# Kernel optimization log

Measured on AMD Instinct MI355X. Metric: run time of the kernel, lower is better.

The kernel has to match this reference:

```python
import jax, jax.numpy as jnp
import numpy as np

TEMPERATURE = 0.07
TAU_THRESHOLD = 0.5

B, D, K = 32768, 512, 2048


def _l2_normalize(x, axis=-1, eps=1e-12):
    # matches torch F.normalize: x / max(||x||, eps)
    n = jnp.linalg.norm(x, axis=axis, keepdims=True)
    return x / jnp.maximum(n, eps)


def setup_inputs() -> dict:
    key = jax.random.key(0)
    k1, k2, k3, k4 = jax.random.split(key, 4)
    embeddings = jax.random.normal(k1, (B, D), dtype=jnp.float32)
    best_similarity = jax.random.uniform(k2, (B,), dtype=jnp.float32)
    global_prototypes = jax.random.normal(k3, (K, D), dtype=jnp.float32)
    prototype_confidence = jax.random.uniform(k4, (K,), dtype=jnp.float32)
    return {
        "embeddings": embeddings,
        "best_similarity": best_similarity,
        "global_prototypes": global_prototypes,
        "prototype_confidence": prototype_confidence,
    }


def reference(embeddings, best_similarity, global_prototypes, prototype_confidence):
    en = _l2_normalize(embeddings, axis=1)          # [B, D]
    pn = _l2_normalize(global_prototypes, axis=1)   # [K, D]
    sims = jnp.einsum("bd,kd->bk", en, pn)          # [B, K] cosine sims
    best_proto_idx = jnp.argmax(sims, axis=1)       # [B]

    logits = sims / TEMPERATURE
    log_probs = jax.nn.log_softmax(logits, axis=1)  # [B, K]
    probs = jnp.exp(log_probs)
    entropy = -jnp.sum(probs * log_probs, axis=1)   # [B]
    max_entropy = jnp.log(jnp.float32(K))
    entropy_norm = entropy / (max_entropy + 1e-8)
    tau_adaptive = TAU_THRESHOLD - 0.2 * entropy_norm

    # confidence_weighted gating
    batch_conf = prototype_confidence[best_proto_idx]                     # [B]
    sigmoid_gate = jax.nn.sigmoid((best_similarity - tau_adaptive) / TEMPERATURE)
    gate = batch_conf * sigmoid_gate                                      # [B]

    target_protos = pn[best_proto_idx]                                    # [B, D]
    dist = jnp.linalg.norm(en - target_protos, axis=1)                    # [B]
    L_proto = jnp.mean(gate * dist)
    return (L_proto, gate)
```

## Files before the change

kernel.cpp:

```cpp
#include <hip/hip_runtime.h>
#include <math.h>


#define NB 32768
#define ND 512
#define NK 2048
#define TEMPR 0.07f
#define INV_T 14.285714285714286f
#define DX 1.4285714e-4f

typedef unsigned short u16;
typedef unsigned long long u64;
using bf16x8 = __attribute__((ext_vector_type(8))) short;
using u16x8 = __attribute__((ext_vector_type(8))) unsigned short;
using f32x16 = __attribute__((ext_vector_type(16))) float;

__device__ inline u16 bf_hi(float x) {
  unsigned u = __float_as_uint(x);
  u = u + 0x7FFFu + ((u >> 16) & 1u);
  return (u16)(u >> 16);
}
__device__ inline float bf_tof(u16 h) {
  return __uint_as_float(((unsigned)h) << 16);
}
__device__ inline void gload_lds16(const void* g, void* l) {
  __builtin_amdgcn_global_load_lds((const __attribute__((address_space(1))) void*)g,
                                   (__attribute__((address_space(3))) void*)l, 16, 0, 0);
}
#define MF(a, b, c) __builtin_amdgcn_mfma_f32_32x32x16_bf16((a), (b), (c), 0, 0, 0)

#define WAIT_LGKM0 { asm volatile("s_waitcnt lgkmcnt(0)" ::: "memory"); \
                     __builtin_amdgcn_sched_barrier(0); }
#define WAIT_VM5   { asm volatile("s_waitcnt vmcnt(5)" ::: "memory"); \
                     __builtin_amdgcn_sched_barrier(0); }
#define SBAR       { __builtin_amdgcn_s_barrier(); \
                     __builtin_amdgcn_sched_barrier(0); }

__global__ __launch_bounds__(256) void kprep_p(const float* __restrict__ P,
                                               u16* __restrict__ Phi,
                                               u16* __restrict__ Plo,
                                               float* __restrict__ invp,
                                               int* __restrict__ cnt) {
  if (blockIdx.x == 0 && threadIdx.x == 0) *cnt = 0;
  const int lane = threadIdx.x & 63, w = threadIdx.x >> 6;
  const int p = blockIdx.x * 4 + w;
  const float4* pr = (const float4*)(P + (size_t)p * ND);
  float4 a = pr[2 * lane], b = pr[2 * lane + 1];
  float ss = a.x * a.x + a.y * a.y + a.z * a.z + a.w * a.w
           + b.x * b.x + b.y * b.y + b.z * b.z + b.w * b.w;
#pragma unroll
  for (int off = 32; off > 0; off >>= 1) ss += __shfl_xor(ss, off);
  const float inv = 1.0f / fmaxf(sqrtf(ss), 1e-12f);
  if (lane == 0) invp[p] = inv;
  u16x8 h8, l8;
#define PCNV(j, f) { float n_ = (f) * inv; u16 hb_ = bf_hi(n_); \
  h8[j] = hb_; l8[j] = bf_hi(n_ - bf_tof(hb_)); }
  PCNV(0, a.x) PCNV(1, a.y) PCNV(2, a.z) PCNV(3, a.w)
  PCNV(4, b.x) PCNV(5, b.y) PCNV(6, b.z) PCNV(7, b.w)
#undef PCNV
  const int kt = p >> 8, pl = p & 255;
  const size_t idx =
      ((size_t)((kt * 32 + (lane >> 1)) * 2 + (lane & 1)) * 256 + pl) * 8;
  *(u16x8*)(Phi + idx) = h8;
  *(u16x8*)(Plo + idx) = l8;
}

__global__ __launch_bounds__(256) void kprep_e2(const float* __restrict__ E,
                                                u16* __restrict__ Ehi,
                                                u16* __restrict__ Elo) {
  const int lane = threadIdx.x & 63, w = threadIdx.x >> 6;
  const int row = blockIdx.x * 4 + w;
  const float4* er = (const float4*)(E + (size_t)row * ND);
  float4 a = er[lane], b = er[lane + 64];
  float ss = a.x * a.x + a.y * a.y + a.z * a.z + a.w * a.w
           + b.x * b.x + b.y * b.y + b.z * b.z + b.w * b.w;
#pragma unroll
  for (int off = 32; off > 0; off >>= 1) ss += __shfl_xor(ss, off);
  const float inv = 1.0f / fmaxf(sqrtf(ss), 1e-12f);
  ushort4 h4, l4;
#define PCNV(dst_h, dst_l, f) { float n_ = (f) * inv; u16 hb_ = bf_hi(n_); \
  dst_h = hb_; dst_l = bf_hi(n_ - bf_tof(hb_)); }
  PCNV(h4.x, l4.x, a.x) PCNV(h4.y, l4.y, a.y) PCNV(h4.z, l4.z, a.z) PCNV(h4.w, l4.w, a.w)
  *(ushort4*)(Ehi + (size_t)row * ND + lane * 4) = h4;
  *(ushort4*)(Elo + (size_t)row * ND + lane * 4) = l4;
  PCNV(h4.x, l4.x, b.x) PCNV(h4.y, l4.y, b.y) PCNV(h4.z, l4.z, b.z) PCNV(h4.w, l4.w, b.w)
  *(ushort4*)(Ehi + (size_t)row * ND + (lane + 64) * 4) = h4;
  *(ushort4*)(Elo + (size_t)row * ND + (lane + 64) * 4) = l4;
#undef PCNV
}

#define UPD2S(i, vv, pp) { \
  float x_ = fmaf((vv), INV_T, -INV_T); \
  float e_ = __expf(x_); \
  sS[i] += e_; uS[i] = fmaf(x_, e_, uS[i]); \
  bool u1_ = x_ > mm1[i]; \
  float lo_ = u1_ ? mm1[i] : x_; \
  mm2[i] = fmaxf(mm2[i], lo_); \
  mm1[i] = u1_ ? x_ : mm1[i]; \
  ixx[i] = u1_ ? (pp) : ixx[i]; }

__global__ __launch_bounds__(256, 3) void kmain_v9(
    const float* __restrict__ BS,
    const u16* __restrict__ PhiG, const u16* __restrict__ PloG,
    const u16* __restrict__ EhiG, const u16* __restrict__ EloG,
    const float* __restrict__ CONF,
    float* __restrict__ tau_ws, float* __restrict__ gd, float* __restrict__ gate_out,
    int* __restrict__ cnt, int* __restrict__ flags, u64* __restrict__ pk) {
  __shared__ u16 Ahi[2][4096], Alo[2][4096];
  __shared__ u16 Bhi[2][1024], Blo[2][1024];

  const int t = threadIdx.x;
  const int lane = t & 63;
  const int w = t >> 6;
  const int wr = w & 1;
  const int wc = w >> 1;
  const int c = lane & 31, h = lane >> 5;
  const int swz = (blockIdx.x & 7) * 64 + (blockIdx.x >> 3);
  const int row0 = swz * 64;

  int aoff[2];
#pragma unroll
  for (int i = 0; i < 2; ++i) aoff[i] = ((w * 2 + i) * 64 + lane) * 8;

  const u16* Bsrc = ((w < 2) ? EhiG : EloG) + (size_t)(row0 + lane) * ND + (w & 1) * 8;
  const int bslot = ((w & 1) * 64 + lane) * 8;

  const int arb = (h * 256 + wr * 128 + c) * 8;
  const int bro = (h * 64 + wc * 32 + c) * 8;

  f32x16 acc0, acc1, acc2, acc3;
#pragma unroll
  for (int i = 0; i < 16; ++i) { acc0[i] = 0.f; acc1[i] = 0.f; acc2[i] = 0.f; acc3[i] = 0.f; }
  float sS[4], uS[4], mm1[4], mm2[4];
  int ixx[4];
#pragma unroll
  for (int i = 0; i < 4; ++i) {
    sS[i] = 0.f; uS[i] = 0.f; mm1[i] = -3.0e38f; mm2[i] = -3.0e38f; ixx[i] = 0;
  }

#define SA9(tile_u16, nx) { \
  _Pragma("unroll") \
  for (int i = 0; i < 2; ++i) { \
    gload_lds16(PhiG + (tile_u16) + aoff[i], &Ahi[nx][aoff[i]]); \
    gload_lds16(PloG + (tile_u16) + aoff[i], &Alo[nx][aoff[i]]); \
  } }
#define SB9(col, nx) { \
  if (w < 2) { gload_lds16(Bsrc + (col), &Bhi[nx][bslot]); } \
  else       { gload_lds16(Bsrc + (col), &Blo[nx][bslot]); } }

  SA9(0, 0);
  SB9(0, 0);
  SA9(4096, 1);
  SB9(16, 1);
  WAIT_VM5;
  SBAR;

#pragma unroll 2
  for (int step = 0; step < 256; ++step) {
    const int cur = step & 1;
    const bf16x8 bh = *(const bf16x8*)&Bhi[cur][bro];
    const bf16x8 bl = *(const bf16x8*)&Blo[cur][bro];
    const bf16x8 ah0 = *(const bf16x8*)&Ahi[cur][arb];
    const bf16x8 ah1 = *(const bf16x8*)&Ahi[cur][arb + 256];
    const bf16x8 ah2 = *(const bf16x8*)&Ahi[cur][arb + 512];
    const bf16x8 ah3 = *(const bf16x8*)&Ahi[cur][arb + 768];
    const bf16x8 al0 = *(const bf16x8*)&Alo[cur][arb];
    const bf16x8 al1 = *(const bf16x8*)&Alo[cur][arb + 256];
    const bf16x8 al2 = *(const bf16x8*)&Alo[cur][arb + 512];
    const bf16x8 al3 = *(const bf16x8*)&Alo[cur][arb + 768];

    acc0 = MF(ah0, bh, acc0); acc1 = MF(ah1, bh, acc1);
    acc2 = MF(ah2, bh, acc2); acc3 = MF(ah3, bh, acc3);

    WAIT_LGKM0;
    SBAR;

    const int ns = (step < 254) ? step + 2 : 255;
    SA9(ns * 4096, cur);
    SB9((ns & 31) * 16, cur);

    acc0 = MF(ah0, bl, acc0); acc1 = MF(ah1, bl, acc1);
    acc2 = MF(ah2, bl, acc2); acc3 = MF(ah3, bl, acc3);
    acc0 = MF(al0, bh, acc0); acc1 = MF(al1, bh, acc1);
    acc2 = MF(al2, bh, acc2); acc3 = MF(al3, bh, acc3);

    if ((step & 31) == 31) {
      const int pb = (step >> 5) * 256 + wr * 128 + 4 * h;
#define DIG(i, ACC) { \
  _Pragma("unroll") \
  for (int r = 0; r < 16; ++r) { \
    UPD2S(i, ACC[r], pb + (i)*32 + (r & 3) + 8 * (r >> 2)) \
    ACC[r] = 0.f; \
  } }
      DIG(0, acc0)
      DIG(1, acc1)
      DIG(2, acc2)
      DIG(3, acc3)
#undef DIG
    }

    WAIT_VM5;
    SBAR;
  }

  __syncthreads();

  float s = 0.f, u = 0.f, m = -3.0e38f, m2f = -3.0e38f;
  int idx = 0;
#pragma unroll
  for (int i = 0; i < 4; ++i) {
    s += sS[i]; u += uS[i];
    bool up = (mm1[i] > m) || (mm1[i] == m && ixx[i] < idx);
    m2f = fmaxf(m2f, mm2[i]);
    m2f = fmaxf(m2f, up ? m : mm1[i]);
    m = up ? mm1[i] : m;
    idx = up ? ixx[i] : idx;
  }

  {
    float mo = __shfl_xor(m, 32);
    float so = __shfl_xor(s, 32);
    float uo = __shfl_xor(u, 32);
    float m2o = __shfl_xor(m2f, 32);
    int io = __shfl_xor(idx, 32);
    s += so; u += uo;
    bool up = (mo > m) || (mo == m && io < idx);
    m2f = fmaxf(m2f, m2o);
    m2f = fmaxf(m2f, up ? m : mo);
    m = up ? mo : m;
    idx = up ? io : idx;
  }

  float* mg = (float*)&Ahi[0][0];
  if (lane < 32) {
    const int base = ((wc * 2 + wr) * 32 + c) * 6;
    mg[base + 0] = m;
    mg[base + 1] = s;
    mg[base + 2] = u;
    mg[base + 3] = __int_as_float(idx);
    mg[base + 4] = m2f;
  }
  __syncthreads();

  if (wr == 0 && lane < 32) {
    const int b0 = ((wc * 2 + 0) * 32 + lane) * 6;
    const int b1 = ((wc * 2 + 1) * 32 + lane) * 6;
    float m1a = mg[b0], s0 = mg[b0 + 1], u0 = mg[b0 + 2];
    int i0 = __float_as_int(mg[b0 + 3]);
    float m2a = mg[b0 + 4];
    float m1b = mg[b1], s1 = mg[b1 + 1], u1 = mg[b1 + 2];
    int i1 = __float_as_int(mg[b1 + 3]);
    float m2b = mg[b1 + 4];

    bool up = (m1b > m1a) || (m1b == m1a && i1 < i0);
    float mf = fmaxf(m1a, m1b);
    float m2ff = fmaxf(fmaxf(m2a, m2b), fminf(m1a, m1b));
    int idxf = up ? i1 : i0;
    bool flg = (mf - m2ff) < DX;
    float sf = s0 + s1, uf = u0 + u1;

    float ent = logf(sf) - uf / sf;
    float tau = 0.5f - 0.2f * (ent * (1.0f / (7.6246190071f + 1e-8f)));
    float simmax = fmaf(mf, TEMPR, 1.0f);
    float dist = sqrtf(fmaxf(2.0f - 2.0f * simmax, 0.0f));
    int grow = row0 + wc * 32 + lane;
    float g = CONF[idxf] / (1.0f + __expf(-(BS[grow] - tau) * INV_T));
    gate_out[grow] = g;
    gd[grow] = g * dist;
    tau_ws[grow] = tau;
    if (flg) {
      pk[grow] = 0ull;
      int p = atomicAdd(cnt, 1);
      flags[p] = grow;
    }
  }
}

__global__ __launch_bounds__(256) void krescore4(
    const float* __restrict__ E, const float* __restrict__ P,
    const float* __restrict__ invp, const int* __restrict__ cnt,
    const int* __restrict__ flags, u64* __restrict__ pk) {
  const int n = *cnt;
  const int total = n * 16;
  const int t = threadIdx.x;
  const int k = t & 15;
  const int G = t >> 4;

  for (int ch = blockIdx.x; ch < total; ch += gridDim.x) {
    const int j = ch >> 4, q = ch & 15;
    const int row = flags[j];
    float4 e[8];
    float ss = 0.f;
    const float4* er = (const float4*)(E + (size_t)row * ND);
#pragma unroll
    for (int i = 0; i < 8; ++i) {
      e[i] = er[k + 16 * i];
      ss += e[i].x * e[i].x + e[i].y * e[i].y + e[i].z * e[i].z + e[i].w * e[i].w;
    }
#pragma unroll
    for (int o = 1; o < 16; o <<= 1) ss += __shfl_xor(ss, o);
    const float inv = 1.0f / fmaxf(sqrtf(ss), 1e-12f);
#pragma unroll
    for (int i = 0; i < 8; ++i) {
      e[i].x *= inv; e[i].y *= inv; e[i].z *= inv; e[i].w *= inv;
    }

    float best = -3.0e38f;
    int bidx = NK;
#pragma unroll 2
    for (int m = 0; m < 8; ++m) {
      const int p = q * 128 + G + 16 * m;
      const float4* pr = (const float4*)(P + (size_t)p * ND);
      float dot = 0.f;
#pragma unroll
      for (int i = 0; i < 8; ++i) {
        float4 a = pr[k + 16 * i];
        dot = fmaf(a.x, e[i].x, dot); dot = fmaf(a.y, e[i].y, dot);
        dot = fmaf(a.z, e[i].z, dot); dot = fmaf(a.w, e[i].w, dot);
      }
#pragma unroll
      for (int o = 1; o < 16; o <<= 1) dot += __shfl_xor(dot, o);
      float sim = dot * invp[p];
      if (sim > best) { best = sim; bidx = p; }
    }
    if (k == 0) {
      unsigned u = __float_as_uint(best);
      unsigned ord = (u & 0x80000000u) ? ~u : (u | 0x80000000u);
      u64 v = ((u64)ord << 32) | (unsigned)(NK - bidx);
      atomicMax(pk + row, v);
    }
  }
}

__global__ __launch_bounds__(1024) void kreduce2(
    float* __restrict__ gd, const float* __restrict__ BS,
    const float* __restrict__ CONF, const float* __restrict__ tau_ws,
    const int* __restrict__ cnt, const int* __restrict__ flags,
    const u64* __restrict__ pk, float* __restrict__ out0,
    float* __restrict__ gate_out) {
  __shared__ float red[1024];
  const int t = threadIdx.x;

  const int n = *cnt;
  for (int j = t; j < n; j += 1024) {
    const int row = flags[j];
    const u64 v = pk[row];
    const unsigned hi = (unsigned)(v >> 32);
    const int idx = NK - (int)(v & 0xFFFFFFFFu);
    const float sim = (hi & 0x80000000u) ? __uint_as_float(hi & 0x7FFFFFFFu)
                                         : __uint_as_float(~hi);
    const float tau = tau_ws[row];
    const float dist = sqrtf(fmaxf(2.0f - 2.0f * sim, 0.0f));
    const float g = CONF[idx] / (1.0f + __expf(-(BS[row] - tau) * INV_T));
    gate_out[row] = g;
    gd[row] = g * dist;
  }
  __syncthreads();

  float s = 0.f;
  const float4* g4 = (const float4*)gd;
  for (int i = t; i < 8192; i += 1024) {
    float4 v = g4[i];
    s += (v.x + v.y) + (v.z + v.w);
  }
  red[t] = s;
  __syncthreads();
  for (int off = 512; off > 0; off >>= 1) {
    if (t < off) red[t] += red[t + off];
    __syncthreads();
  }
  if (t == 0) out0[0] = red[0] * (1.0f / 32768.0f);
}

extern "C" void kernel_launch(void* const* d_in, const int* in_sizes, int n_in,
                              void* d_out, int out_size, void* d_ws, size_t ws_size,
                              hipStream_t stream) {
  const float* E = (const float*)d_in[0];
  const float* BS = (const float*)d_in[1];
  const float* P = (const float*)d_in[2];
  const float* CONF = (const float*)d_in[3];
  float* out = (float*)d_out;

  char* wsb = (char*)d_ws;
  u16* Phi = (u16*)wsb;
  u16* Plo = (u16*)(wsb + ((size_t)2 << 20));
  u16* Ehi = (u16*)(wsb + ((size_t)4 << 20));
  u16* Elo = (u16*)(wsb + ((size_t)36 << 20));
  char* tail = wsb + ((size_t)68 << 20);
  float* tau_ws = (float*)tail;
  float* gd = (float*)(tail + 131072);
  int* flags = (int*)(tail + 2 * 131072);
  int* cnt = (int*)(tail + 3 * 131072);
  float* invp = (float*)(tail + 3 * 131072 + 4096);
  u64* pk = (u64*)(tail + 3 * 131072 + 4096 + 8192);

  kprep_p<<<512, 256, 0, stream>>>(P, Phi, Plo, invp, cnt);
  kprep_e2<<<8192, 256, 0, stream>>>(E, Ehi, Elo);
  kmain_v9<<<512, 256, 0, stream>>>(BS, Phi, Plo, Ehi, Elo, CONF, tau_ws, gd,
                                    out + 1, cnt, flags, pk);
  krescore4<<<2048, 256, 0, stream>>>(E, P, invp, cnt, flags, pk);
  kreduce2<<<1, 1024, 0, stream>>>(gd, BS, CONF, tau_ws, cnt, flags, pk,
                                   out, out + 1);
}
```

Before: 280.5 us.

## Split prototype dimension across two blocks and convert embeddings to bf16 in-kernel

The main GEMM kernel now splits the 2048 prototypes into two halves, launching 1024 blocks instead of 512. Each block writes partial softmax/argmax statistics, and a new merge kernel combines them and computes the gate. The embedding prep kernel now only computes inverse norms. The main kernel loads fp32 embeddings directly and converts them to hi/lo bf16 pairs into LDS each step, which removes the 64MB Ehi/Elo round-trip through global memory. In exchange it adds an extra launch, partial-result traffic, and VALU conversion work in the inner loop, and the embedding tile is reconverted by both halves.

```diff
diff --git a/kernel.cpp b/kernel.cpp
--- a/kernel.cpp
+++ b/kernel.cpp
@@ -65,9 +65,8 @@
   *(u16x8*)(Plo + idx) = l8;
 }
 
-__global__ __launch_bounds__(256) void kprep_e2(const float* __restrict__ E,
-                                                u16* __restrict__ Ehi,
-                                                u16* __restrict__ Elo) {
+__global__ __launch_bounds__(256) void kprep_e(const float* __restrict__ E,
+                                               float* __restrict__ inv_e) {
   const int lane = threadIdx.x & 63, w = threadIdx.x >> 6;
   const int row = blockIdx.x * 4 + w;
   const float4* er = (const float4*)(E + (size_t)row * ND);
@@ -76,17 +75,7 @@
            + b.x * b.x + b.y * b.y + b.z * b.z + b.w * b.w;
 #pragma unroll
   for (int off = 32; off > 0; off >>= 1) ss += __shfl_xor(ss, off);
-  const float inv = 1.0f / fmaxf(sqrtf(ss), 1e-12f);
-  ushort4 h4, l4;
-#define PCNV(dst_h, dst_l, f) { float n_ = (f) * inv; u16 hb_ = bf_hi(n_); \
-  dst_h = hb_; dst_l = bf_hi(n_ - bf_tof(hb_)); }
-  PCNV(h4.x, l4.x, a.x) PCNV(h4.y, l4.y, a.y) PCNV(h4.z, l4.z, a.z) PCNV(h4.w, l4.w, a.w)
-  *(ushort4*)(Ehi + (size_t)row * ND + lane * 4) = h4;
-  *(ushort4*)(Elo + (size_t)row * ND + lane * 4) = l4;
-  PCNV(h4.x, l4.x, b.x) PCNV(h4.y, l4.y, b.y) PCNV(h4.z, l4.z, b.z) PCNV(h4.w, l4.w, b.w)
-  *(ushort4*)(Ehi + (size_t)row * ND + (lane + 64) * 4) = h4;
-  *(ushort4*)(Elo + (size_t)row * ND + (lane + 64) * 4) = l4;
-#undef PCNV
+  if (lane == 0) inv_e[row] = 1.0f / fmaxf(sqrtf(ss), 1e-12f);
 }
 
 #define UPD2S(i, vv, pp) { \
@@ -99,13 +88,10 @@
   mm1[i] = u1_ ? x_ : mm1[i]; \
   ixx[i] = u1_ ? (pp) : ixx[i]; }
 
-__global__ __launch_bounds__(256, 3) void kmain_v9(
-    const float* __restrict__ BS,
+__global__ __launch_bounds__(256, 3) void kmain_v10(
+    const float* __restrict__ E, const float* __restrict__ inv_e,
     const u16* __restrict__ PhiG, const u16* __restrict__ PloG,
-    const u16* __restrict__ EhiG, const u16* __restrict__ EloG,
-    const float* __restrict__ CONF,
-    float* __restrict__ tau_ws, float* __restrict__ gd, float* __restrict__ gate_out,
-    int* __restrict__ cnt, int* __restrict__ flags, u64* __restrict__ pk) {
+    float4* __restrict__ partA, float* __restrict__ partB) {
   __shared__ u16 Ahi[2][4096], Alo[2][4096];
   __shared__ u16 Bhi[2][1024], Blo[2][1024];
 
@@ -115,15 +101,18 @@
   const int wr = w & 1;
   const int wc = w >> 1;
   const int c = lane & 31, h = lane >> 5;
-  const int swz = (blockIdx.x & 7) * 64 + (blockIdx.x >> 3);
-  const int row0 = swz * 64;
+  const int swz = (blockIdx.x & 7) * 128 + (blockIdx.x >> 3);
+  const int rt = swz >> 1, kh = swz & 1;
+  const int row0 = rt * 64;
 
   int aoff[2];
 #pragma unroll
   for (int i = 0; i < 2; ++i) aoff[i] = ((w * 2 + i) * 64 + lane) * 8;
-
-  const u16* Bsrc = ((w < 2) ? EhiG : EloG) + (size_t)(row0 + lane) * ND + (w & 1) * 8;
-  const int bslot = ((w & 1) * 64 + lane) * 8;
+  const int abase = kh * 128 * 4096;
+
+  const float* Brow = E + (size_t)(row0 + lane) * ND + w * 4;
+  const float inve = inv_e[row0 + lane];
+  const int bws = ((w >> 1) * 64 + lane) * 8 + (w & 1) * 4;
 
   const int arb = (h * 256 + wr * 128 + c) * 8;
   const int bro = (h * 64 + wc * 32 + c) * 8;
@@ -138,25 +127,38 @@
     sS[i] = 0.f; uS[i] = 0.f; mm1[i] = -3.0e38f; mm2[i] = -3.0e38f; ixx[i] = 0;
   }
 
-#define SA9(tile_u16, nx) { \
+#define SA10(tile_u16, nx) { \
   _Pragma("unroll") \
   for (int i = 0; i < 2; ++i) { \
-    gload_lds16(PhiG + (tile_u16) + aoff[i], &Ahi[nx][aoff[i]]); \
-    gload_lds16(PloG + (tile_u16) + aoff[i], &Alo[nx][aoff[i]]); \
+    gload_lds16(PhiG + abase + (tile_u16) + aoff[i], &Ahi[nx][aoff[i]]); \
+    gload_lds16(PloG + abase + (tile_u16) + aoff[i], &Alo[nx][aoff[i]]); \
   } }
-#define SB9(col, nx) { \
-  if (w < 2) { gload_lds16(Bsrc + (col), &Bhi[nx][bslot]); } \
-  else       { gload_lds16(Bsrc + (col), &Blo[nx][bslot]); } }
-
-  SA9(0, 0);
-  SB9(0, 0);
-  SA9(4096, 1);
-  SB9(16, 1);
+#define BCNV(v) { ushort4 h4, l4; float n_; u16 hb_; \
+  n_ = (v).x * inve; hb_ = bf_hi(n_); h4.x = hb_; l4.x = bf_hi(n_ - bf_tof(hb_)); \
+  n_ = (v).y * inve; hb_ = bf_hi(n_); h4.y = hb_; l4.y = bf_hi(n_ - bf_tof(hb_)); \
+  n_ = (v).z * inve; hb_ = bf_hi(n_); h4.z = hb_; l4.z = bf_hi(n_ - bf_tof(hb_)); \
+  n_ = (v).w * inve; hb_ = bf_hi(n_); h4.w = hb_; l4.w = bf_hi(n_ - bf_tof(hb_)); \
+  *(ushort4*)&Bhi[cur][bws] = h4; *(ushort4*)&Blo[cur][bws] = l4; }
+
+  {
+    const int cur = 0;
+    float4 v = *(const float4*)(Brow + 0 * 16);
+    BCNV(v)
+  }
+  {
+    const int cur = 1;
+    float4 v = *(const float4*)(Brow + 1 * 16);
+    BCNV(v)
+  }
+  SA10(0 * 4096, 0);
+  float4 bstg = *(const float4*)(Brow + 2 * 16);
+  SA10(1 * 4096, 1);
   WAIT_VM5;
+  WAIT_LGKM0;
   SBAR;
 
 #pragma unroll 2
-  for (int step = 0; step < 256; ++step) {
+  for (int step = 0; step < 128; ++step) {
     const int cur = step & 1;
     const bf16x8 bh = *(const bf16x8*)&Bhi[cur][bro];
     const bf16x8 bl = *(const bf16x8*)&Blo[cur][bro];
@@ -175,9 +177,11 @@
     WAIT_LGKM0;
     SBAR;
 
-    const int ns = (step < 254) ? step + 2 : 255;
-    SA9(ns * 4096, cur);
-    SB9((ns & 31) * 16, cur);
+    BCNV(bstg)
+    const int nb = (step < 125) ? step + 3 : 127;
+    bstg = *(const float4*)(Brow + (size_t)(nb & 31) * 16);
+    const int ns = (step < 126) ? step + 2 : 127;
+    SA10(ns * 4096, cur);
 
     acc0 = MF(ah0, bl, acc0); acc1 = MF(ah1, bl, acc1);
     acc2 = MF(ah2, bl, acc2); acc3 = MF(ah3, bl, acc3);
@@ -185,7 +189,7 @@
     acc2 = MF(al2, bh, acc2); acc3 = MF(al3, bh, acc3);
 
     if ((step & 31) == 31) {
-      const int pb = (step >> 5) * 256 + wr * 128 + 4 * h;
+      const int pb = (kh * 4 + (step >> 5)) * 256 + wr * 128 + 4 * h;
 #define DIG(i, ACC) { \
   _Pragma("unroll") \
   for (int r = 0; r < 16; ++r) { \
@@ -256,23 +260,47 @@
     float mf = fmaxf(m1a, m1b);
     float m2ff = fmaxf(fmaxf(m2a, m2b), fminf(m1a, m1b));
     int idxf = up ? i1 : i0;
-    bool flg = (mf - m2ff) < DX;
     float sf = s0 + s1, uf = u0 + u1;
 
-    float ent = logf(sf) - uf / sf;
-    float tau = 0.5f - 0.2f * (ent * (1.0f / (7.6246190071f + 1e-8f)));
-    float simmax = fmaf(mf, TEMPR, 1.0f);
-    float dist = sqrtf(fmaxf(2.0f - 2.0f * simmax, 0.0f));
-    int grow = row0 + wc * 32 + lane;
-    float g = CONF[idxf] / (1.0f + __expf(-(BS[grow] - tau) * INV_T));
-    gate_out[grow] = g;
-    gd[grow] = g * dist;
-    tau_ws[grow] = tau;
-    if (flg) {
-      pk[grow] = 0ull;
-      int p = atomicAdd(cnt, 1);
-      flags[p] = grow;
-    }
+    const int grow = row0 + wc * 32 + lane;
+    partA[(grow << 1) | kh] = make_float4(mf, sf, uf, __int_as_float(idxf));
+    partB[(grow << 1) | kh] = m2ff;
+  }
+}
+
+__global__ __launch_bounds__(256) void kmerge(
+    const float4* __restrict__ partA, const float* __restrict__ partB,
+    const float* __restrict__ BS, const float* __restrict__ CONF,
+    float* __restrict__ tau_ws, float* __restrict__ gd,
+    float* __restrict__ gate_out, int* __restrict__ cnt,
+    int* __restrict__ flags, u64* __restrict__ pk) {
+  const int row = blockIdx.x * 256 + threadIdx.x;
+  float4 a = partA[row * 2], b = partA[row * 2 + 1];
+  float m2a = partB[row * 2], m2b = partB[row * 2 + 1];
+  float m1a = a.x, s0 = a.y, u0 = a.z;
+  int i0 = __float_as_int(a.w);
+  float m1b = b.x, s1 = b.y, u1 = b.z;
+  int i1 = __float_as_int(b.w);
+
+  bool up = m1b > m1a;
+  float m = fmaxf(m1a, m1b);
+  float m2f = fmaxf(fmaxf(m2a, m2b), fminf(m1a, m1b));
+  int idx = up ? i1 : i0;
+  bool flg = (m - m2f) < DX;
+  float s = s0 + s1, u = u0 + u1;
+
+  float ent = logf(s) - u / s;
+  float tau = 0.5f - 0.2f * (ent * (1.0f / (7.6246190071f + 1e-8f)));
+  float simmax = fmaf(m, TEMPR, 1.0f);
+  float dist = sqrtf(fmaxf(2.0f - 2.0f * simmax, 0.0f));
+  float g = CONF[idx] / (1.0f + __expf(-(BS[row] - tau) * INV_T));
+  gate_out[row] = g;
+  gd[row] = g * dist;
+  tau_ws[row] = tau;
+  if (flg) {
+    pk[row] = 0ull;
+    int p = atomicAdd(cnt, 1);
+    flags[p] = row;
   }
 }
 
@@ -384,20 +412,22 @@
   char* wsb = (char*)d_ws;
   u16* Phi = (u16*)wsb;
   u16* Plo = (u16*)(wsb + ((size_t)2 << 20));
-  u16* Ehi = (u16*)(wsb + ((size_t)4 << 20));
-  u16* Elo = (u16*)(wsb + ((size_t)36 << 20));
-  char* tail = wsb + ((size_t)68 << 20);
-  float* tau_ws = (float*)tail;
-  float* gd = (float*)(tail + 131072);
-  int* flags = (int*)(tail + 2 * 131072);
-  int* cnt = (int*)(tail + 3 * 131072);
-  float* invp = (float*)(tail + 3 * 131072 + 4096);
-  u64* pk = (u64*)(tail + 3 * 131072 + 4096 + 8192);
+  char* tail = wsb + ((size_t)4 << 20);
+  float* inv_e = (float*)tail;
+  float* tau_ws = (float*)(tail + 131072);
+  float* gd = (float*)(tail + 2 * 131072);
+  int* flags = (int*)(tail + 3 * 131072);
+  int* cnt = (int*)(tail + 4 * 131072);
+  float* invp = (float*)(tail + 4 * 131072 + 4096);
+  u64* pk = (u64*)(tail + 4 * 131072 + 12288);
+  float4* partA = (float4*)(tail + ((size_t)1 << 20));
+  float* partB = (float*)(tail + ((size_t)2 << 20));
 
   kprep_p<<<512, 256, 0, stream>>>(P, Phi, Plo, invp, cnt);
-  kprep_e2<<<8192, 256, 0, stream>>>(E, Ehi, Elo);
-  kmain_v9<<<512, 256, 0, stream>>>(BS, Phi, Plo, Ehi, Elo, CONF, tau_ws, gd,
-                                    out + 1, cnt, flags, pk);
+  kprep_e<<<8192, 256, 0, stream>>>(E, inv_e);
+  kmain_v10<<<1024, 256, 0, stream>>>(E, inv_e, Phi, Plo, partA, partB);
+  kmerge<<<128, 256, 0, stream>>>(partA, partB, BS, CONF, tau_ws, gd, out + 1,
+                                  cnt, flags, pk);
   krescore4<<<2048, 256, 0, stream>>>(E, P, invp, cnt, flags, pk);
   kreduce2<<<1, 1024, 0, stream>>>(gd, BS, CONF, tau_ws, cnt, flags, pk,
                                    out, out + 1);
```

Measured after the change: 283.2 us. Within noise of the previous version (+0.9%).
